# Kernel tuning notes

Measured on AMD Instinct MI355X. Metric: run time of the kernel, lower is better.

The kernel has to match this reference:

```python
import jax, jax.numpy as jnp
import numpy as np

N_NODES = 100000
N_EDGES = 1600000
D = 8                      # node_channels_in = [D, D]
PROD = D * D               # 64
MSG_DIM = 128
IN_MSG = 2 * PROD + 2 * 2 + 2 * 1   # 134
MSG_OUT = 2 * D            # 16
IN_EIG = 2 * D + 2 * D     # node_channels_sum + 2*D = 32


def setup_inputs() -> dict:
    key = jax.random.key(0)
    ks = jax.random.split(key, 12)
    a = jax.random.normal(ks[0], (N_NODES, D, D), dtype=jnp.float32)
    h_i = 0.5 * (a + jnp.swapaxes(a, -1, -2))  # symmetric so eigh is valid
    edge_index = jax.random.randint(ks[1], (2, N_EDGES), 0, N_NODES)
    node_params = jax.random.normal(ks[2], (N_NODES, 2), dtype=jnp.float32)
    edge_params = jax.random.normal(ks[3], (N_EDGES, 1), dtype=jnp.float32)
    s = 0.05
    return {
        "h_i": h_i,
        "node_params": node_params,
        "edge_params": edge_params,
        "W1": jax.random.normal(ks[4], (IN_MSG, MSG_DIM), dtype=jnp.float32) * s,
        "b1": jnp.zeros((MSG_DIM,), dtype=jnp.float32),
        "W2": jax.random.normal(ks[5], (MSG_DIM, MSG_OUT), dtype=jnp.float32) * s,
        "b2": jnp.zeros((MSG_OUT,), dtype=jnp.float32),
        "W3": jax.random.normal(ks[6], (IN_EIG, MSG_DIM), dtype=jnp.float32) * s,
        "b3": jnp.zeros((MSG_DIM,), dtype=jnp.float32),
        "W4": jax.random.normal(ks[7], (MSG_DIM, D), dtype=jnp.float32) * s,
        "b4": jnp.zeros((D,), dtype=jnp.float32),
        "edge_index": edge_index,
    }


def reference(h_i, node_params, edge_params, W1, b1, W2, b2, W3, b3, W4, b4, edge_index):
    sender = edge_index[0]
    receiver = edge_index[1]
    E = sender.shape[0]
    N = node_params.shape[0]

    # gather + flatten node states per edge: [E, D*D]
    h_s = h_i[sender].reshape(E, -1)
    h_r = h_i[receiver].reshape(E, -1)
    # faithful to torch: edge_params[edge_index] -> [2, E, 1] then view(E, -1) -> [E, 2]
    ep = edge_params[edge_index].reshape(E, -1)

    cat = jnp.concatenate(
        [h_s, h_r, node_params[sender], node_params[receiver], ep], axis=1
    )  # [E, 134]

    # phi_message_Real: Linear -> SiLU -> Linear -> SiLU
    hidden = jax.nn.silu(cat @ W1 + b1)          # [E, 128]
    I_ij = jax.nn.silu(hidden @ W2 + b2)         # [E, 16]

    # scatter_add over receiver
    agg = jax.ops.segment_sum(I_ij, receiver, num_segments=N)  # [N, 16]

    # eigh-based update
    eigvals, eigvecs = jnp.linalg.eigh(h_i)          # [N, D], [N, D, D]
    mags = jnp.linalg.norm(eigvecs, axis=-1)         # [N, D] (row norms, as torch.norm(dim=-1))

    feats = jnp.concatenate([agg, eigvals, mags], axis=1)  # [N, 32]
    lam = jax.nn.softmax(jax.nn.silu(feats @ W3 + b3) @ W4 + b4, axis=-1)  # [N, D]

    # V diag(lam) V^T  per node
    h_updated = jnp.einsum("nij,nj,nkj->nik", eigvecs, lam, eigvecs)
    return h_updated
```

## Files before the change

kernel.cpp:

```cpp
#include <hip/hip_runtime.h>
#include <math.h>

typedef __attribute__((ext_vector_type(8))) short bf16x8;
typedef __attribute__((ext_vector_type(4))) float f32x4;
typedef _Float16 half2v __attribute__((ext_vector_type(2)));
typedef _Float16 f16x8 __attribute__((ext_vector_type(8)));

__device__ __forceinline__ float silu(float x) {
    return x / (1.0f + __expf(-x));
}

__device__ __forceinline__ unsigned short f2bf(float x) {
    union { float f; unsigned u; } v; v.f = x;
    unsigned r = v.u + 0x7fffu + ((v.u >> 16) & 1u);
    return (unsigned short)(r >> 16);
}

__device__ __forceinline__ unsigned pack2(float a, float b) {
    return (unsigned)f2bf(a) | ((unsigned)f2bf(b) << 16);
}

__device__ __forceinline__ unsigned pack2h(float a, float b) {
    half2v h; h[0] = (_Float16)a; h[1] = (_Float16)b;
    return __builtin_bit_cast(unsigned, h);
}

__device__ __forceinline__ unsigned cvt_pk(float lo, float hi) {
    unsigned r;
    asm("v_cvt_pk_bf16_f32 %0, %1, %2" : "=v"(r) : "v"(lo), "v"(hi));
    return r;
}

__global__ __launch_bounds__(256)
void k_pre2(const float* __restrict__ h_i,
            const float* __restrict__ np,
            const float* __restrict__ ep,
            const int* __restrict__ eidx,
            const float* __restrict__ W1, const float* __restrict__ b1,
            unsigned short* __restrict__ SAB,
            unsigned* __restrict__ epk,
            int N, int E)
{
    if (blockIdx.x >= 1024) {
        const int tid = (blockIdx.x - 1024) * 256 + threadIdx.x;
        const int gs = 512 * 256;
        for (int i = tid; i < E; i += gs)
            epk[i] = pack2h(ep[eidx[2 * i]], ep[eidx[2 * i + 1]]);
        return;
    }

    const int t = threadIdx.x;
    const int lane = t & 63;
    const int wv = t >> 6;
    const int lr = lane & 15;
    const int lq = lane >> 4;

    bf16x8 aw[4][3];
    #pragma unroll
    for (int mf = 0; mf < 4; ++mf) {
        const int c = wv * 64 + mf * 16 + lr;
        const bool isA = c < 128;
        const int col = c & 127;
        #pragma unroll
        for (int ks = 0; ks < 3; ++ks) {
            bf16x8 w;
            #pragma unroll
            for (int j = 0; j < 8; ++j) {
                const int kl = lq * 8 + j;
                float v = 0.0f;
                if (ks < 2) {
                    const int kk = ks * 32 + kl;
                    v = W1[(size_t)(isA ? kk : 64 + kk) * 128 + col];
                } else if (kl < 2) {
                    v = W1[(size_t)((isA ? 128 : 130) + kl) * 128 + col];
                }
                w[j] = (short)f2bf(v);
            }
            aw[mf][ks] = w;
        }
    }
    float4 b1v[4];
    #pragma unroll
    for (int mf = 0; mf < 4; ++mf) {
        if (wv < 2) b1v[mf] = *(const float4*)&b1[wv * 64 + mf * 16 + lq * 4];
        else        b1v[mf] = make_float4(0.f, 0.f, 0.f, 0.f);
    }

    const int nTiles = (N + 15) / 16;
    for (int tile = blockIdx.x; tile < nTiles; tile += 1024) {
        const int n  = tile * 16 + lr;
        const int nc = (n < N) ? n : (N - 1);

        const float* hr = h_i + (size_t)nc * 64;
        bf16x8 B0, B1, B2;
        {
            float4 a0 = *(const float4*)&hr[lq * 8];
            float4 a1 = *(const float4*)&hr[lq * 8 + 4];
            float4 a2 = *(const float4*)&hr[32 + lq * 8];
            float4 a3 = *(const float4*)&hr[32 + lq * 8 + 4];
            unsigned u[4];
            u[0] = pack2(a0.x, a0.y); u[1] = pack2(a0.z, a0.w);
            u[2] = pack2(a1.x, a1.y); u[3] = pack2(a1.z, a1.w);
            B0 = __builtin_bit_cast(bf16x8, *(uint4*)u);
            u[0] = pack2(a2.x, a2.y); u[1] = pack2(a2.z, a2.w);
            u[2] = pack2(a3.x, a3.y); u[3] = pack2(a3.z, a3.w);
            B1 = __builtin_bit_cast(bf16x8, *(uint4*)u);
            unsigned z[4] = {0u, 0u, 0u, 0u};
            if (lq == 0) z[0] = pack2(np[2 * nc], np[2 * nc + 1]);
            B2 = __builtin_bit_cast(bf16x8, *(uint4*)z);
        }

        f32x4 acc[4];
        #pragma unroll
        for (int mf = 0; mf < 4; ++mf) {
            acc[mf] = (f32x4){0.f, 0.f, 0.f, 0.f};
            acc[mf] = __builtin_amdgcn_mfma_f32_16x16x32_bf16(aw[mf][0], B0, acc[mf], 0, 0, 0);
            acc[mf] = __builtin_amdgcn_mfma_f32_16x16x32_bf16(aw[mf][1], B1, acc[mf], 0, 0, 0);
            acc[mf] = __builtin_amdgcn_mfma_f32_16x16x32_bf16(aw[mf][2], B2, acc[mf], 0, 0, 0);
        }

        if (n < N) {
            unsigned short* row = SAB + (size_t)n * 256;
            #pragma unroll
            for (int mf = 0; mf < 4; ++mf) {
                uint2 u;
                u.x = pack2h(acc[mf][0] + b1v[mf].x, acc[mf][1] + b1v[mf].y);
                u.y = pack2h(acc[mf][2] + b1v[mf].z, acc[mf][3] + b1v[mf].w);
                *(uint2*)&row[wv * 64 + mf * 16 + lq * 4] = u;
            }
        }
    }
}

__global__ __launch_bounds__(256, 3)
void k_edge_v5(const unsigned short* __restrict__ SAB,
               const unsigned* __restrict__ epk,
               const int* __restrict__ eidx,
               const float* __restrict__ W1,
               const float* __restrict__ W2, const float* __restrict__ b2,
               float* __restrict__ agg,
               int N, int E)
{
    const int t = threadIdx.x;
    const int lane = t & 63;
    const int wv = t >> 6;
    const int lr = lane & 15;
    const int lq = lane >> 4;

    half2v wA[4][4], wB[4][4];
    #pragma unroll
    for (int ks = 0; ks < 4; ++ks)
        #pragma unroll
        for (int c = 0; c < 4; ++c) {
            const int d = ks * 32 + lq * 8 + 2 * c;
            half2v a; a[0] = (_Float16)W1[132 * 128 + d]; a[1] = (_Float16)W1[132 * 128 + d + 1];
            half2v b; b[0] = (_Float16)W1[133 * 128 + d]; b[1] = (_Float16)W1[133 * 128 + d + 1];
            wA[ks][c] = a; wB[ks][c] = b;
        }

    bf16x8 bw2[4];
    #pragma unroll
    for (int ks = 0; ks < 4; ++ks) {
        bf16x8 w;
        #pragma unroll
        for (int j = 0; j < 8; ++j) {
            const int k = ks * 32 + lq * 8 + j;
            w[j] = (short)f2bf(W2[(size_t)k * 16 + lr]);
        }
        bw2[ks] = w;
    }
    const float bias2 = b2[lr];

    const uint4* S4 = (const uint4*)SAB;
    const int nG = (E + 15) / 16;
    const int gstride = gridDim.x * 4;
    int g = blockIdx.x * 4 + wv;
    if (g >= nG) return;

    int s0, r0; unsigned ep0; int rc0[4];
    uint4 A0[4], B0[4];
    {
        const int eb = g * 16;
        const int e = eb + lr; const int ec = (e < E) ? e : (E - 1);
        s0 = eidx[ec]; r0 = eidx[E + ec]; ep0 = epk[ec];
        if (eb + 16 <= E) {
            const int4 rv = *(const int4*)&eidx[E + eb + lq * 4];
            rc0[0] = rv.x; rc0[1] = rv.y; rc0[2] = rv.z; rc0[3] = rv.w;
        } else {
            #pragma unroll
            for (int r2 = 0; r2 < 4; ++r2) {
                int e4 = eb + lq * 4 + r2;
                rc0[r2] = eidx[E + ((e4 < E) ? e4 : (E - 1))];
            }
        }
        const uint4* pa = S4 + (size_t)s0 * 32;
        const uint4* pb = S4 + (size_t)r0 * 32 + 16;
        #pragma unroll
        for (int ks = 0; ks < 4; ++ks) { A0[ks] = pa[ks * 4 + lq]; B0[ks] = pb[ks * 4 + lq]; }
    }

    for (; g < nG; g += gstride) {
        const int gn = g + gstride;
        const bool hn = gn < nG;

        int s1 = 0, r1 = 0; unsigned ep1 = 0; int rc1[4] = {0, 0, 0, 0};
        if (hn) {
            const int eb = gn * 16;
            const int e = eb + lr; const int ec = (e < E) ? e : (E - 1);
            s1 = eidx[ec]; r1 = eidx[E + ec]; ep1 = epk[ec];
            if (eb + 16 <= E) {
                const int4 rv = *(const int4*)&eidx[E + eb + lq * 4];
                rc1[0] = rv.x; rc1[1] = rv.y; rc1[2] = rv.z; rc1[3] = rv.w;
            } else {
                #pragma unroll
                for (int r2 = 0; r2 < 4; ++r2) {
                    int e4 = eb + lq * 4 + r2;
                    rc1[r2] = eidx[E + ((e4 < E) ? e4 : (E - 1))];
                }
            }
        }

        const unsigned elo = (ep0 & 0xffffu) | (ep0 << 16);
        const unsigned ehi = (ep0 >> 16) | (ep0 & 0xffff0000u);
        const half2v e0 = __builtin_bit_cast(half2v, elo);
        const half2v e1 = __builtin_bit_cast(half2v, ehi);

        bf16x8 af[4];
        #pragma unroll
        for (int ks = 0; ks < 4; ++ks) {
            unsigned w[4];
            const unsigned* ua = (const unsigned*)&A0[ks];
            const unsigned* ub = (const unsigned*)&B0[ks];
            #pragma unroll
            for (int c = 0; c < 4; ++c) {
                half2v v = __builtin_bit_cast(half2v, ua[c])
                         + __builtin_bit_cast(half2v, ub[c]);
                v = wA[ks][c] * e0 + v;
                v = wB[ks][c] * e1 + v;
                const float x0 = (float)v[0];
                const float x1 = (float)v[1];
                w[c] = cvt_pk(silu(x0), silu(x1));
            }
            af[ks] = __builtin_bit_cast(bf16x8, *(uint4*)w);
        }

        uint4 A1[4], B1[4];
        if (hn) {
            const uint4* pa = S4 + (size_t)s1 * 32;
            const uint4* pb = S4 + (size_t)r1 * 32 + 16;
            #pragma unroll
            for (int ks = 0; ks < 4; ++ks) { A1[ks] = pa[ks * 4 + lq]; B1[ks] = pb[ks * 4 + lq]; }
        }

        f32x4 acc = (f32x4){0.f, 0.f, 0.f, 0.f};
        #pragma unroll
        for (int ks = 0; ks < 4; ++ks)
            acc = __builtin_amdgcn_mfma_f32_16x16x32_bf16(af[ks], bw2[ks], acc, 0, 0, 0);

        const int eb = g * 16;
        if (eb + 16 <= E) {
            #pragma unroll
            for (int r2 = 0; r2 < 4; ++r2)
                atomicAdd(&agg[(size_t)rc0[r2] * 16 + lr], silu(acc[r2] + bias2));
        } else {
            #pragma unroll
            for (int r2 = 0; r2 < 4; ++r2)
                if (eb + lq * 4 + r2 < E)
                    atomicAdd(&agg[(size_t)rc0[r2] * 16 + lr], silu(acc[r2] + bias2));
        }

        if (hn) {
            s0 = s1; r0 = r1; ep0 = ep1;
            #pragma unroll
            for (int r2 = 0; r2 < 4; ++r2) rc0[r2] = rc1[r2];
            #pragma unroll
            for (int ks = 0; ks < 4; ++ks) { A0[ks] = A1[ks]; B0[ks] = B1[ks]; }
        }
    }
}

__host__ __device__ constexpr int tix(int i, int j) {
    return (i <= j) ? (i * 8 - (i * (i + 1)) / 2 + j)
                    : (j * 8 - (j * (j + 1)) / 2 + i);
}

template <int P, int Q>
__device__ __forceinline__ void jrot(float* T, float* V) {
    const float app = T[tix(P, P)];
    const float aqq = T[tix(Q, Q)];
    const float apq = T[tix(P, Q)];

    float theta = (aqq - app) / (2.0f * apq);
    float at = fabsf(theta);
    float tt = 1.0f / (at + sqrtf(at * at + 1.0f));
    tt = (theta < 0.0f) ? -tt : tt;
    float cc = __frsqrt_rn(tt * tt + 1.0f);
    float ss = tt * cc;

    const bool skip = !(fabsf(apq) > 1e-36f);
    const float c  = skip ? 1.0f : cc;
    const float s  = skip ? 0.0f : ss;
    const float tu = skip ? 0.0f : tt;

    #pragma unroll
    for (int k = 0; k < 8; ++k) {
        if (k == P || k == Q) continue;
        const float akp = T[tix(k, P)], akq = T[tix(k, Q)];
        T[tix(k, P)] = c * akp - s * akq;
        T[tix(k, Q)] = s * akp + c * akq;
    }
    T[tix(P, P)] = app - tu * apq;
    T[tix(Q, Q)] = aqq + tu * apq;
    T[tix(P, Q)] = 0.0f;

    #pragma unroll
    for (int k = 0; k < 8; ++k) {
        const float vp = V[k * 8 + P], vq = V[k * 8 + Q];
        V[k * 8 + P] = c * vp - s * vq;
        V[k * 8 + Q] = s * vp + c * vq;
    }
}

__device__ __forceinline__ void jacobi_sweep(float* T, float* V) {
    jrot<0,1>(T,V); jrot<0,2>(T,V); jrot<0,3>(T,V); jrot<0,4>(T,V);
    jrot<0,5>(T,V); jrot<0,6>(T,V); jrot<0,7>(T,V);
    jrot<1,2>(T,V); jrot<1,3>(T,V); jrot<1,4>(T,V); jrot<1,5>(T,V);
    jrot<1,6>(T,V); jrot<1,7>(T,V);
    jrot<2,3>(T,V); jrot<2,4>(T,V); jrot<2,5>(T,V); jrot<2,6>(T,V);
    jrot<2,7>(T,V);
    jrot<3,4>(T,V); jrot<3,5>(T,V); jrot<3,6>(T,V); jrot<3,7>(T,V);
    jrot<4,5>(T,V); jrot<4,6>(T,V); jrot<4,7>(T,V);
    jrot<5,6>(T,V); jrot<5,7>(T,V);
    jrot<6,7>(T,V);
}

#define CSWAP(a, b)                                                          \
    {                                                                        \
        bool sw = eig[a] > eig[b];                                           \
        float lo = sw ? eig[b] : eig[a];                                     \
        float hi = sw ? eig[a] : eig[b];                                     \
        eig[a] = lo; eig[b] = hi;                                            \
        _Pragma("unroll")                                                    \
        for (int k = 0; k < 8; ++k) {                                        \
            float va = V[k * 8 + a], vb = V[k * 8 + b];                      \
            V[k * 8 + a] = sw ? vb : va;                                     \
            V[k * 8 + b] = sw ? va : vb;                                     \
        }                                                                    \
    }

__global__ __launch_bounds__(256)
void k_node2(const float* __restrict__ h_i,
             const float* __restrict__ agg,
             const float* __restrict__ W3, const float* __restrict__ b3,
             const float* __restrict__ W4, const float* __restrict__ b4,
             float* __restrict__ out, int N)
{
    __shared__ _Float16 fl[4][64][40];
    __shared__ _Float16 hl[4][16][136];
    __shared__ float    zl[4][64][8];

    const int t = threadIdx.x;
    const int lane = t & 63;
    const int wv = t >> 6;
    const int lr = lane & 15;
    const int lq = lane >> 4;

    const int n  = blockIdx.x * 256 + t;
    const int nc = (n < N) ? n : (N - 1);

    float T[36], V[64];
    {
        float A[64];
        const float4* src = (const float4*)(h_i + (size_t)nc * 64);
        #pragma unroll
        for (int i = 0; i < 16; ++i) ((float4*)A)[i] = src[i];
        #pragma unroll
        for (int i = 0; i < 8; ++i)
            #pragma unroll
            for (int j = 0; j < 8; ++j)
                if (i <= j) T[tix(i, j)] = A[i * 8 + j];
    }
    #pragma unroll
    for (int i = 0; i < 64; ++i) V[i] = 0.0f;
    #pragma unroll
    for (int i = 0; i < 8; ++i) V[i * 8 + i] = 1.0f;

    #pragma unroll 1
    for (int sw = 0; sw < 5; ++sw) jacobi_sweep(T, V);

    float eig[8];
    #pragma unroll
    for (int i = 0; i < 8; ++i) eig[i] = T[tix(i, i)];

    CSWAP(0,1) CSWAP(2,3) CSWAP(4,5) CSWAP(6,7)
    CSWAP(0,2) CSWAP(1,3) CSWAP(4,6) CSWAP(5,7)
    CSWAP(1,2) CSWAP(5,6)
    CSWAP(0,4) CSWAP(1,5) CSWAP(2,6) CSWAP(3,7)
    CSWAP(2,4) CSWAP(3,5)
    CSWAP(1,2) CSWAP(3,4) CSWAP(5,6)

    f16x8 w3f[8];
    #pragma unroll
    for (int nf = 0; nf < 8; ++nf) {
        f16x8 w;
        #pragma unroll
        for (int j = 0; j < 8; ++j)
            w[j] = (_Float16)W3[(size_t)(lq * 8 + j) * 128 + nf * 16 + lr];
        w3f[nf] = w;
    }
    f16x8 w4f[4];
    #pragma unroll
    for (int ks = 0; ks < 4; ++ks) {
        f16x8 w;
        #pragma unroll
        for (int j = 0; j < 8; ++j)
            w[j] = (lr < 8) ? (_Float16)W4[(size_t)(ks * 32 + lq * 8 + j) * 8 + lr]
                            : (_Float16)0.0f;
        w4f[ks] = w;
    }
    float b3v[8];
    #pragma unroll
    for (int nf = 0; nf < 8; ++nf) b3v[nf] = b3[nf * 16 + lr];
    const float b4v = (lr < 8) ? b4[lr] : 0.0f;

    {
        float f[32];
        const float4* ag = (const float4*)(agg + (size_t)nc * 16);
        #pragma unroll
        for (int i = 0; i < 4; ++i) {
            float4 v = ag[i];
            f[i * 4 + 0] = v.x; f[i * 4 + 1] = v.y;
            f[i * 4 + 2] = v.z; f[i * 4 + 3] = v.w;
        }
        #pragma unroll
        for (int i = 0; i < 8; ++i) f[16 + i] = eig[i];
        #pragma unroll
        for (int i = 0; i < 8; ++i) f[24 + i] = 1.0f;

        unsigned* dst = (unsigned*)&fl[wv][lane][0];
        #pragma unroll
        for (int i = 0; i < 16; ++i) dst[i] = pack2h(f[2 * i], f[2 * i + 1]);
    }
    __syncthreads();

    #pragma unroll 1
    for (int b = 0; b < 4; ++b) {
        const f16x8 a1 = *(const f16x8*)&fl[wv][b * 16 + lr][lq * 8];
        f32x4 acc1[8];
        #pragma unroll
        for (int nf = 0; nf < 8; ++nf) {
            acc1[nf] = (f32x4){0.f, 0.f, 0.f, 0.f};
            acc1[nf] = __builtin_amdgcn_mfma_f32_16x16x32_f16(a1, w3f[nf], acc1[nf], 0, 0, 0);
        }
        #pragma unroll
        for (int nf = 0; nf < 8; ++nf)
            #pragma unroll
            for (int r2 = 0; r2 < 4; ++r2) {
                const float x = acc1[nf][r2] + b3v[nf];
                hl[wv][lq * 4 + r2][nf * 16 + lr] = (_Float16)silu(x);
            }
        __syncthreads();

        f32x4 acc2 = (f32x4){0.f, 0.f, 0.f, 0.f};
        #pragma unroll
        for (int ks = 0; ks < 4; ++ks) {
            const f16x8 a2 = *(const f16x8*)&hl[wv][lr][ks * 32 + lq * 8];
            acc2 = __builtin_amdgcn_mfma_f32_16x16x32_f16(a2, w4f[ks], acc2, 0, 0, 0);
        }
        if (lr < 8) {
            #pragma unroll
            for (int r2 = 0; r2 < 4; ++r2)
                zl[wv][b * 16 + lq * 4 + r2][lr] = acc2[r2] + b4v;
        }
        __syncthreads();
    }

    float z[8];
    {
        float4 z0 = *(const float4*)&zl[wv][lane][0];
        float4 z1 = *(const float4*)&zl[wv][lane][4];
        z[0] = z0.x; z[1] = z0.y; z[2] = z0.z; z[3] = z0.w;
        z[4] = z1.x; z[5] = z1.y; z[6] = z1.z; z[7] = z1.w;
    }
    float m = z[0];
    #pragma unroll
    for (int o = 1; o < 8; ++o) m = fmaxf(m, z[o]);
    float lam[8], den = 0.0f;
    #pragma unroll
    for (int o = 0; o < 8; ++o) { lam[o] = __expf(z[o] - m); den += lam[o]; }
    const float inv = 1.0f / den;
    #pragma unroll
    for (int o = 0; o < 8; ++o) lam[o] *= inv;

    if (n < N) {
        float* orow = out + (size_t)n * 64;
        #pragma unroll
        for (int i = 0; i < 8; ++i) {
            float si[8];
            #pragma unroll
            for (int j = 0; j < 8; ++j) si[j] = lam[j] * V[i * 8 + j];
            float r[8];
            #pragma unroll
            for (int k = 0; k < 8; ++k) {
                float sum = 0.0f;
                #pragma unroll
                for (int j = 0; j < 8; ++j) sum += si[j] * V[k * 8 + j];
                r[k] = sum;
            }
            ((float4*)orow)[i * 2 + 0] = make_float4(r[0], r[1], r[2], r[3]);
            ((float4*)orow)[i * 2 + 1] = make_float4(r[4], r[5], r[6], r[7]);
        }
    }
}

#define CATS 168
#define HS   136
__global__ __launch_bounds__(256, 2)
void k_edge_v2(const float* __restrict__ h_i,
               const float* __restrict__ node_params,
               const float* __restrict__ edge_params,
               const float* __restrict__ W1, const float* __restrict__ b1,
               const float* __restrict__ W2, const float* __restrict__ b2,
               const int* __restrict__ eidx,
               float* __restrict__ agg,
               int N, int E)
{
    __shared__ unsigned short smem[23680];
    unsigned short* w1t = smem;
    unsigned short* w2t = smem + 128 * CATS;
    unsigned short* cat = smem;
    unsigned short* hid = smem + 64 * CATS;

    const int t = threadIdx.x;
    const int lane = t & 63;
    const int wv = t >> 6;
    const int wn = wv & 1;
    const int wm = wv >> 1;
    const int lr = lane & 15;
    const int lq = lane >> 4;

    for (int idx = t; idx < 128 * 80; idx += 256) {
        const int col = idx & 127, kp = idx >> 7;
        const int k0 = 2 * kp;
        float f0 = (k0     < 134) ? W1[(size_t)k0       * 128 + col] : 0.0f;
        float f1 = (k0 + 1 < 134) ? W1[(size_t)(k0 + 1) * 128 + col] : 0.0f;
        *(unsigned*)&w1t[col * CATS + k0] = pack2(f0, f1);
    }
    for (int idx = t; idx < 16 * 64; idx += 256) {
        const int col = idx & 15, kp = idx >> 4;
        const int k0 = 2 * kp;
        *(unsigned*)&w2t[col * HS + k0] =
            pack2(W2[(size_t)k0 * 16 + col], W2[(size_t)(k0 + 1) * 16 + col]);
    }
    __syncthreads();

    bf16x8 bw1[4][5];
    #pragma unroll
    for (int nf = 0; nf < 4; ++nf)
        #pragma unroll
        for (int ks = 0; ks < 5; ++ks)
            bw1[nf][ks] = *(const bf16x8*)&w1t[(wn * 64 + nf * 16 + lr) * CATS + ks * 32 + lq * 8];
    bf16x8 bw2[4];
    #pragma unroll
    for (int ks = 0; ks < 4; ++ks)
        bw2[ks] = *(const bf16x8*)&w2t[lr * HS + ks * 32 + lq * 8];

    float bias1[4];
    #pragma unroll
    for (int nf = 0; nf < 4; ++nf) bias1[nf] = b1[wn * 64 + nf * 16 + lr];
    const float bias2 = b2[lr];
    __syncthreads();

    const int el = t >> 2;
    const int p  = t & 3;

    const int nTiles = E / 64;
    for (int tile = blockIdx.x; tile < nTiles; tile += gridDim.x) {
        const int ebase = tile * 64;
        {
            const int eg  = ebase + el;
            const int egc = (eg < E) ? eg : (E - 1);
            const int s = eidx[egc];
            const int r = eidx[E + egc];
            const float4* hs = (const float4*)(h_i + (size_t)s * 64);
            const float4* hr = (const float4*)(h_i + (size_t)r * 64);
            unsigned short* crow = cat + el * CATS;
            #pragma unroll
            for (int m = 0; m < 8; ++m) {
                const int q = p + 4 * m;
                float4 v = (q < 16) ? hs[q] : hr[q - 16];
                uint2 u; u.x = pack2(v.x, v.y); u.y = pack2(v.z, v.w);
                *(uint2*)&crow[q * 4] = u;
            }
            if (p == 0) {
                const int i0 = eidx[2 * egc];
                const int i1 = eidx[2 * egc + 1];
                uint4 u;
                u.x = pack2(node_params[2 * s], node_params[2 * s + 1]);
                u.y = pack2(node_params[2 * r], node_params[2 * r + 1]);
                u.z = pack2(edge_params[i0], edge_params[i1]);
                u.w = 0u;
                *(uint4*)&crow[128] = u;
            } else {
                uint4 z; z.x = z.y = z.z = z.w = 0u;
                *(uint4*)&crow[136 + (p - 1) * 8] = z;
            }
        }
        __syncthreads();

        f32x4 acc[2][4];
        #pragma unroll
        for (int mf = 0; mf < 2; ++mf)
            #pragma unroll
            for (int nf = 0; nf < 4; ++nf)
                acc[mf][nf] = (f32x4){0.f, 0.f, 0.f, 0.f};

        const unsigned short* pa = cat + (wm * 32 + lr) * CATS + lq * 8;
        #pragma unroll
        for (int ks = 0; ks < 5; ++ks) {
            const bf16x8 a0 = *(const bf16x8*)(pa + ks * 32);
            const bf16x8 a1 = *(const bf16x8*)(pa + 16 * CATS + ks * 32);
            #pragma unroll
            for (int nf = 0; nf < 4; ++nf) {
                acc[0][nf] = __builtin_amdgcn_mfma_f32_16x16x32_bf16(a0, bw1[nf][ks], acc[0][nf], 0, 0, 0);
                acc[1][nf] = __builtin_amdgcn_mfma_f32_16x16x32_bf16(a1, bw1[nf][ks], acc[1][nf], 0, 0, 0);
            }
        }
        __syncthreads();

        #pragma unroll
        for (int mf = 0; mf < 2; ++mf)
            #pragma unroll
            for (int nf = 0; nf < 4; ++nf) {
                const float bb = bias1[nf];
                #pragma unroll
                for (int r2 = 0; r2 < 4; ++r2) {
                    const float x = acc[mf][nf][r2] + bb;
                    hid[(wm * 32 + mf * 16 + lq * 4 + r2) * HS + wn * 64 + nf * 16 + lr] =
                        f2bf(silu(x));
                }
            }
        __syncthreads();

        f32x4 acc2 = (f32x4){0.f, 0.f, 0.f, 0.f};
        const unsigned short* ph = hid + (wv * 16 + lr) * HS + lq * 8;
        #pragma unroll
        for (int ks = 0; ks < 4; ++ks)
            acc2 = __builtin_amdgcn_mfma_f32_16x16x32_bf16(
                *(const bf16x8*)(ph + ks * 32), bw2[ks], acc2, 0, 0, 0);

        #pragma unroll
        for (int r2 = 0; r2 < 4; ++r2) {
            const int eg2 = ebase + wv * 16 + lq * 4 + r2;
            if (eg2 < E) {
                const int rcv = eidx[E + eg2];
                const float v = silu(acc2[r2] + bias2);
                atomicAdd(&agg[(size_t)rcv * 16 + lr], v);
            }
        }
        __syncthreads();
    }
}

extern "C" void kernel_launch(void* const* d_in, const int* in_sizes, int n_in,
                              void* d_out, int out_size, void* d_ws, size_t ws_size,
                              hipStream_t stream) {
    const float* h_i  = (const float*)d_in[0];
    const float* npar = (const float*)d_in[1];
    const float* epar = (const float*)d_in[2];
    const float* W1   = (const float*)d_in[3];
    const float* b1   = (const float*)d_in[4];
    const float* W2   = (const float*)d_in[5];
    const float* b2   = (const float*)d_in[6];
    const float* W3   = (const float*)d_in[7];
    const float* b3   = (const float*)d_in[8];
    const float* W4   = (const float*)d_in[9];
    const float* b4   = (const float*)d_in[10];
    const int*   eidx = (const int*)d_in[11];

    const int N = in_sizes[0] / 64;
    const int E = in_sizes[11] / 2;

    const size_t aggB = (size_t)N * 16 * sizeof(float);
    size_t off = (aggB + 255) & ~(size_t)255;
    const size_t sabOff = off;                  off += (size_t)N * 256 * 2;
    off = (off + 255) & ~(size_t)255;
    const size_t epkOff = off;                  off += (size_t)E * 4;
    const size_t need = off;

    float* agg = (float*)d_ws;
    hipMemsetAsync(agg, 0, aggB, stream);

    if (ws_size >= need) {
        unsigned short* SAB = (unsigned short*)((char*)d_ws + sabOff);
        unsigned* epk = (unsigned*)((char*)d_ws + epkOff);

        k_pre2<<<1536, 256, 0, stream>>>(h_i, npar, epar, eidx, W1, b1,
                                         SAB, epk, N, E);
        k_edge_v5<<<2048, 256, 0, stream>>>(SAB, epk, eidx, W1, W2, b2,
                                            agg, N, E);
    } else {
        int blocks = E / 64;
        if (blocks > 768) blocks = 768;
        k_edge_v2<<<blocks, 256, 0, stream>>>(h_i, npar, epar, W1, b1, W2, b2,
                                              eidx, agg, N, E);
    }
    k_node2<<<(N + 255) / 256, 256, 0, stream>>>(h_i, agg, W3, b3, W4, b4,
                                                 (float*)d_out, N);
}
```

Before: 285.6 us.

## Overlap Jacobi eigensolve with edge kernel via extra blocks, stash eigenvectors in output

Moves the per-node Jacobi eigendecomposition out of the node kernel and into extra blocks appended to the edge-MLP launch. The edge work is memory and atomic bound and the eigensolve is ALU bound, so running them together is meant to overlap the two. Eigenvectors are written into the output buffer, and the node kernel reads them back and recomputes eigenvalues as V^T A V. This adds a 64-float round trip per node through global memory, and the node kernel reads and writes the same buffer in place. The extra eigen blocks also compete with the edge blocks for occupancy, and the edge kernel is limited by launch bounds to 3 blocks per SM.

```diff
diff --git a/kernel.cpp b/kernel.cpp
--- a/kernel.cpp
+++ b/kernel.cpp
@@ -29,6 +29,118 @@
     unsigned r;
     asm("v_cvt_pk_bf16_f32 %0, %1, %2" : "=v"(r) : "v"(lo), "v"(hi));
     return r;
+}
+
+__host__ __device__ constexpr int tix(int i, int j) {
+    return (i <= j) ? (i * 8 - (i * (i + 1)) / 2 + j)
+                    : (j * 8 - (j * (j + 1)) / 2 + i);
+}
+
+template <int P, int Q>
+__device__ __forceinline__ void jrot(float* T, float* V) {
+    const float app = T[tix(P, P)];
+    const float aqq = T[tix(Q, Q)];
+    const float apq = T[tix(P, Q)];
+
+    float theta = (aqq - app) / (2.0f * apq);
+    float at = fabsf(theta);
+    float tt = 1.0f / (at + sqrtf(at * at + 1.0f));
+    tt = (theta < 0.0f) ? -tt : tt;
+    float cc = __frsqrt_rn(tt * tt + 1.0f);
+    float ss = tt * cc;
+
+    const bool skip = !(fabsf(apq) > 1e-36f);
+    const float c  = skip ? 1.0f : cc;
+    const float s  = skip ? 0.0f : ss;
+    const float tu = skip ? 0.0f : tt;
+
+    #pragma unroll
+    for (int k = 0; k < 8; ++k) {
+        if (k == P || k == Q) continue;
+        const float akp = T[tix(k, P)], akq = T[tix(k, Q)];
+        T[tix(k, P)] = c * akp - s * akq;
+        T[tix(k, Q)] = s * akp + c * akq;
+    }
+    T[tix(P, P)] = app - tu * apq;
+    T[tix(Q, Q)] = aqq + tu * apq;
+    T[tix(P, Q)] = 0.0f;
+
+    #pragma unroll
+    for (int k = 0; k < 8; ++k) {
+        const float vp = V[k * 8 + P], vq = V[k * 8 + Q];
+        V[k * 8 + P] = c * vp - s * vq;
+        V[k * 8 + Q] = s * vp + c * vq;
+    }
+}
+
+__device__ __forceinline__ void jacobi_sweep(float* T, float* V) {
+    jrot<0,1>(T,V); jrot<0,2>(T,V); jrot<0,3>(T,V); jrot<0,4>(T,V);
+    jrot<0,5>(T,V); jrot<0,6>(T,V); jrot<0,7>(T,V);
+    jrot<1,2>(T,V); jrot<1,3>(T,V); jrot<1,4>(T,V); jrot<1,5>(T,V);
+    jrot<1,6>(T,V); jrot<1,7>(T,V);
+    jrot<2,3>(T,V); jrot<2,4>(T,V); jrot<2,5>(T,V); jrot<2,6>(T,V);
+    jrot<2,7>(T,V);
+    jrot<3,4>(T,V); jrot<3,5>(T,V); jrot<3,6>(T,V); jrot<3,7>(T,V);
+    jrot<4,5>(T,V); jrot<4,6>(T,V); jrot<4,7>(T,V);
+    jrot<5,6>(T,V); jrot<5,7>(T,V);
+    jrot<6,7>(T,V);
+}
+
+#define CSWAP(a, b)                                                          \
+    {                                                                        \
+        bool sw = eig[a] > eig[b];                                           \
+        float lo = sw ? eig[b] : eig[a];                                     \
+        float hi = sw ? eig[a] : eig[b];                                     \
+        eig[a] = lo; eig[b] = hi;                                            \
+        _Pragma("unroll")                                                    \
+        for (int k = 0; k < 8; ++k) {                                        \
+            float va = V[k * 8 + a], vb = V[k * 8 + b];                      \
+            V[k * 8 + a] = sw ? vb : va;                                     \
+            V[k * 8 + b] = sw ? va : vb;                                     \
+        }                                                                    \
+    }
+
+__device__ __forceinline__ void eig_node(const float* __restrict__ h_i,
+                                         float* vout, int n, int N)
+{
+    const int nc = (n < N) ? n : (N - 1);
+    float T[36], V[64];
+    {
+        float A[64];
+        const float4* src = (const float4*)(h_i + (size_t)nc * 64);
+        #pragma unroll
+        for (int i = 0; i < 16; ++i) ((float4*)A)[i] = src[i];
+        #pragma unroll
+        for (int i = 0; i < 8; ++i)
+            #pragma unroll
+            for (int j = 0; j < 8; ++j)
+                if (i <= j) T[tix(i, j)] = A[i * 8 + j];
+    }
+    #pragma unroll
+    for (int i = 0; i < 64; ++i) V[i] = 0.0f;
+    #pragma unroll
+    for (int i = 0; i < 8; ++i) V[i * 8 + i] = 1.0f;
+
+    #pragma unroll 1
+    for (int sw = 0; sw < 5; ++sw) jacobi_sweep(T, V);
+
+    float eig[8];
+    #pragma unroll
+    for (int i = 0; i < 8; ++i) eig[i] = T[tix(i, i)];
+
+    CSWAP(0,1) CSWAP(2,3) CSWAP(4,5) CSWAP(6,7)
+    CSWAP(0,2) CSWAP(1,3) CSWAP(4,6) CSWAP(5,7)
+    CSWAP(1,2) CSWAP(5,6)
+    CSWAP(0,4) CSWAP(1,5) CSWAP(2,6) CSWAP(3,7)
+    CSWAP(2,4) CSWAP(3,5)
+    CSWAP(1,2) CSWAP(3,4) CSWAP(5,6)
+
+    if (n < N) {
+        float* row = vout + (size_t)n * 64;
+        #pragma unroll
+        for (int i = 0; i < 16; ++i)
+            ((float4*)row)[i] = make_float4(V[i*4+0], V[i*4+1], V[i*4+2], V[i*4+3]);
+    }
 }
 
 __global__ __launch_bounds__(256)
@@ -133,14 +245,22 @@
 }
 
 __global__ __launch_bounds__(256, 3)
-void k_edge_v5(const unsigned short* __restrict__ SAB,
-               const unsigned* __restrict__ epk,
-               const int* __restrict__ eidx,
-               const float* __restrict__ W1,
-               const float* __restrict__ W2, const float* __restrict__ b2,
-               float* __restrict__ agg,
-               int N, int E)
+void k_edge_v5e(const unsigned short* __restrict__ SAB,
+                const unsigned* __restrict__ epk,
+                const int* __restrict__ eidx,
+                const float* __restrict__ W1,
+                const float* __restrict__ W2, const float* __restrict__ b2,
+                float* __restrict__ agg,
+                const float* __restrict__ h_i,
+                float* vout, int EB,
+                int N, int E)
 {
+    if ((int)blockIdx.x >= EB) {
+        const int n = (blockIdx.x - EB) * 256 + threadIdx.x;
+        eig_node(h_i, vout, n, N);
+        return;
+    }
+
     const int t = threadIdx.x;
     const int lane = t & 63;
     const int wv = t >> 6;
@@ -173,7 +293,7 @@
 
     const uint4* S4 = (const uint4*)SAB;
     const int nG = (E + 15) / 16;
-    const int gstride = gridDim.x * 4;
+    const int gstride = EB * 4;
     int g = blockIdx.x * 4 + wv;
     if (g >= nG) return;
 
@@ -279,81 +399,20 @@
     }
 }
 
-__host__ __device__ constexpr int tix(int i, int j) {
-    return (i <= j) ? (i * 8 - (i * (i + 1)) / 2 + j)
-                    : (j * 8 - (j * (j + 1)) / 2 + i);
-}
-
-template <int P, int Q>
-__device__ __forceinline__ void jrot(float* T, float* V) {
-    const float app = T[tix(P, P)];
-    const float aqq = T[tix(Q, Q)];
-    const float apq = T[tix(P, Q)];
-
-    float theta = (aqq - app) / (2.0f * apq);
-    float at = fabsf(theta);
-    float tt = 1.0f / (at + sqrtf(at * at + 1.0f));
-    tt = (theta < 0.0f) ? -tt : tt;
-    float cc = __frsqrt_rn(tt * tt + 1.0f);
-    float ss = tt * cc;
-
-    const bool skip = !(fabsf(apq) > 1e-36f);
-    const float c  = skip ? 1.0f : cc;
-    const float s  = skip ? 0.0f : ss;
-    const float tu = skip ? 0.0f : tt;
-
-    #pragma unroll
-    for (int k = 0; k < 8; ++k) {
-        if (k == P || k == Q) continue;
-        const float akp = T[tix(k, P)], akq = T[tix(k, Q)];
-        T[tix(k, P)] = c * akp - s * akq;
-        T[tix(k, Q)] = s * akp + c * akq;
-    }
-    T[tix(P, P)] = app - tu * apq;
-    T[tix(Q, Q)] = aqq + tu * apq;
-    T[tix(P, Q)] = 0.0f;
-
-    #pragma unroll
-    for (int k = 0; k < 8; ++k) {
-        const float vp = V[k * 8 + P], vq = V[k * 8 + Q];
-        V[k * 8 + P] = c * vp - s * vq;
-        V[k * 8 + Q] = s * vp + c * vq;
-    }
-}
-
-__device__ __forceinline__ void jacobi_sweep(float* T, float* V) {
-    jrot<0,1>(T,V); jrot<0,2>(T,V); jrot<0,3>(T,V); jrot<0,4>(T,V);
-    jrot<0,5>(T,V); jrot<0,6>(T,V); jrot<0,7>(T,V);
-    jrot<1,2>(T,V); jrot<1,3>(T,V); jrot<1,4>(T,V); jrot<1,5>(T,V);
-    jrot<1,6>(T,V); jrot<1,7>(T,V);
-    jrot<2,3>(T,V); jrot<2,4>(T,V); jrot<2,5>(T,V); jrot<2,6>(T,V);
-    jrot<2,7>(T,V);
-    jrot<3,4>(T,V); jrot<3,5>(T,V); jrot<3,6>(T,V); jrot<3,7>(T,V);
-    jrot<4,5>(T,V); jrot<4,6>(T,V); jrot<4,7>(T,V);
-    jrot<5,6>(T,V); jrot<5,7>(T,V);
-    jrot<6,7>(T,V);
-}
-
-#define CSWAP(a, b)                                                          \
-    {                                                                        \
-        bool sw = eig[a] > eig[b];                                           \
-        float lo = sw ? eig[b] : eig[a];                                     \
-        float hi = sw ? eig[a] : eig[b];                                     \
-        eig[a] = lo; eig[b] = hi;                                            \
-        _Pragma("unroll")                                                    \
-        for (int k = 0; k < 8; ++k) {                                        \
-            float va = V[k * 8 + a], vb = V[k * 8 + b];                      \
-            V[k * 8 + a] = sw ? vb : va;                                     \
-            V[k * 8 + b] = sw ? va : vb;                                     \
-        }                                                                    \
-    }
-
 __global__ __launch_bounds__(256)
-void k_node2(const float* __restrict__ h_i,
-             const float* __restrict__ agg,
-             const float* __restrict__ W3, const float* __restrict__ b3,
-             const float* __restrict__ W4, const float* __restrict__ b4,
-             float* __restrict__ out, int N)
+void k_eig(const float* __restrict__ h_i, float* vout, int N)
+{
+    const int n = blockIdx.x * 256 + threadIdx.x;
+    eig_node(h_i, vout, n, N);
+}
+
+__global__ __launch_bounds__(256)
+void k_node_lite(const float* __restrict__ h_i,
+                 const float* vbuf,
+                 const float* __restrict__ agg,
+                 const float* __restrict__ W3, const float* __restrict__ b3,
+                 const float* __restrict__ W4, const float* __restrict__ b4,
+                 float* out, int N)
 {
     __shared__ _Float16 fl[4][64][40];
     __shared__ _Float16 hl[4][16][136];
@@ -368,36 +427,30 @@
     const int n  = blockIdx.x * 256 + t;
     const int nc = (n < N) ? n : (N - 1);
 
-    float T[36], V[64];
+    float V[64];
+    float eigv[8];
     {
         float A[64];
-        const float4* src = (const float4*)(h_i + (size_t)nc * 64);
-        #pragma unroll
-        for (int i = 0; i < 16; ++i) ((float4*)A)[i] = src[i];
-        #pragma unroll
-        for (int i = 0; i < 8; ++i)
-            #pragma unroll
-            for (int j = 0; j < 8; ++j)
-                if (i <= j) T[tix(i, j)] = A[i * 8 + j];
-    }
-    #pragma unroll
-    for (int i = 0; i < 64; ++i) V[i] = 0.0f;
-    #pragma unroll
-    for (int i = 0; i < 8; ++i) V[i * 8 + i] = 1.0f;
-
-    #pragma unroll 1
-    for (int sw = 0; sw < 5; ++sw) jacobi_sweep(T, V);
-
-    float eig[8];
-    #pragma unroll
-    for (int i = 0; i < 8; ++i) eig[i] = T[tix(i, i)];
-
-    CSWAP(0,1) CSWAP(2,3) CSWAP(4,5) CSWAP(6,7)
-    CSWAP(0,2) CSWAP(1,3) CSWAP(4,6) CSWAP(5,7)
-    CSWAP(1,2) CSWAP(5,6)
-    CSWAP(0,4) CSWAP(1,5) CSWAP(2,6) CSWAP(3,7)
-    CSWAP(2,4) CSWAP(3,5)
-    CSWAP(1,2) CSWAP(3,4) CSWAP(5,6)
+        const float4* sv = (const float4*)(vbuf + (size_t)nc * 64);
+        const float4* sa = (const float4*)(h_i + (size_t)nc * 64);
+        #pragma unroll
+        for (int i = 0; i < 16; ++i) {
+            ((float4*)V)[i] = sv[i];
+            ((float4*)A)[i] = sa[i];
+        }
+        #pragma unroll
+        for (int j = 0; j < 8; ++j) {
+            float acc = 0.0f;
+            #pragma unroll
+            for (int i = 0; i < 8; ++i) {
+                float w = 0.0f;
+                #pragma unroll
+                for (int k = 0; k < 8; ++k) w += A[i * 8 + k] * V[k * 8 + j];
+                acc += V[i * 8 + j] * w;
+            }
+            eigv[j] = acc;
+        }
+    }
 
     f16x8 w3f[8];
     #pragma unroll
@@ -433,7 +486,7 @@
             f[i * 4 + 2] = v.z; f[i * 4 + 3] = v.w;
         }
         #pragma unroll
-        for (int i = 0; i < 8; ++i) f[16 + i] = eig[i];
+        for (int i = 0; i < 8; ++i) f[16 + i] = eigv[i];
         #pragma unroll
         for (int i = 0; i < 8; ++i) f[24 + i] = 1.0f;
 
@@ -689,22 +742,27 @@
     const size_t need = off;
 
     float* agg = (float*)d_ws;
-    hipMemsetAsync(agg, 0, aggB, stream);
+    (void)hipMemsetAsync(agg, 0, aggB, stream);
+
+    const int eigB = (N + 255) / 256;
 
     if (ws_size >= need) {
         unsigned short* SAB = (unsigned short*)((char*)d_ws + sabOff);
         unsigned* epk = (unsigned*)((char*)d_ws + epkOff);
 
+        const int EB = 2048;
         k_pre2<<<1536, 256, 0, stream>>>(h_i, npar, epar, eidx, W1, b1,
                                          SAB, epk, N, E);
-        k_edge_v5<<<2048, 256, 0, stream>>>(SAB, epk, eidx, W1, W2, b2,
-                                            agg, N, E);
+        k_edge_v5e<<<EB + eigB, 256, 0, stream>>>(SAB, epk, eidx, W1, W2, b2,
+                                                  agg, h_i, (float*)d_out, EB,
+                                                  N, E);
     } else {
+        k_eig<<<eigB, 256, 0, stream>>>(h_i, (float*)d_out, N);
         int blocks = E / 64;
         if (blocks > 768) blocks = 768;
         k_edge_v2<<<blocks, 256, 0, stream>>>(h_i, npar, epar, W1, b1, W2, b2,
                                               eidx, agg, N, E);
     }
-    k_node2<<<(N + 255) / 256, 256, 0, stream>>>(h_i, agg, W3, b3, W4, b4,
-                                                 (float*)d_out, N);
-}
+    k_node_lite<<<eigB, 256, 0, stream>>>(h_i, (const float*)d_out, agg,
+                                          W3, b3, W4, b4, (float*)d_out, N);
+}
```

New measurement: 438.3 us. 1.53x slower.
